# Optimization experiments

Measured on AMD Instinct MI355X. Metric: run time of the kernel, lower is better.

## Reference

```python
import jax, jax.numpy as jnp
import numpy as np

B, C, D, H, W = 1, 32, 48, 64, 208
EPS = 1e-5  # BatchNorm eps


def setup_inputs() -> dict:
    key = jax.random.key(0)
    ks = jax.random.split(key, 8)
    x = jax.random.normal(ks[0], (B, C, D, H, W), jnp.float32)
    g = jax.random.normal(ks[1], (B, 20, H, W), jnp.float32)
    conv_w = jax.random.normal(ks[2], (C, C, 3, 3, 3), jnp.float32) * 0.02
    bn1_gamma = 1.0 + 0.1 * jax.random.normal(ks[3], (C,), jnp.float32)
    bn1_beta = 0.1 * jax.random.normal(ks[4], (C,), jnp.float32)
    bn1_mean = 0.1 * jax.random.normal(ks[5], (C,), jnp.float32)
    bn1_var = jax.random.uniform(ks[6], (C,), jnp.float32, 0.5, 1.5)
    bn2_gamma = 1.0 + 0.1 * jax.random.normal(ks[7], (C,), jnp.float32)
    bn2_beta = jnp.zeros((C,), jnp.float32)
    bn2_mean = jnp.zeros((C,), jnp.float32)
    bn2_var = jnp.ones((C,), jnp.float32)
    return {
        'x': x, 'g': g, 'conv_w': conv_w,
        'bn1_gamma': bn1_gamma, 'bn1_beta': bn1_beta, 'bn1_mean': bn1_mean, 'bn1_var': bn1_var,
        'bn2_gamma': bn2_gamma, 'bn2_beta': bn2_beta, 'bn2_mean': bn2_mean, 'bn2_var': bn2_var,
    }


def _l1_normalize(k):
    # F.normalize(k, p=1, dim=1)
    return k / jnp.maximum(jnp.sum(jnp.abs(k), axis=1, keepdims=True), 1e-12)


def _sga_scan(x, w):
    """Directional semi-global aggregation along the LAST axis.
    x: [B,C,D,H,L] cost volume, w: [B,5,H,L] L1-normalized guidance weights.
    Recurrence (GANet SGA):
      A[p,d] = w0*x[p,d] + w1*A[p-1,d] + w2*A[p-1,d-1] + w3*A[p-1,d+1] + w4*max_d' A[p-1,d']
    """
    xs = jnp.moveaxis(x, -1, 0)  # [L,B,C,D,H]
    ws = jnp.moveaxis(w, -1, 0)  # [L,B,5,H]

    def step(prev, inp):
        xi, wi = inp  # [B,C,D,H], [B,5,H]
        w0, w1, w2, w3, w4 = [wi[:, i][:, None, None, :] for i in range(5)]
        up = jnp.concatenate([prev[:, :, :1], prev[:, :, :-1]], axis=2)   # A[d-1]
        dn = jnp.concatenate([prev[:, :, 1:], prev[:, :, -1:]], axis=2)   # A[d+1]
        mx = jnp.max(prev, axis=2, keepdims=True)                          # max_d A
        out = w0 * xi + w1 * prev + w2 * up + w3 * dn + w4 * mx
        return out, out

    _, outs = jax.lax.scan(step, xs[0], (xs, ws))  # boundary: carry init = raw cost slice
    return jnp.moveaxis(outs, 0, -1)


def _sga(x, k1, k2, k3, k4):
    # direction 1: left -> right (along W)
    d1 = _sga_scan(x, k1)
    # direction 2: right -> left
    d2 = jnp.flip(_sga_scan(jnp.flip(x, -1), jnp.flip(k2, -1)), -1)
    # vertical directions: swap H<->W so the scan axis is H
    xv = jnp.swapaxes(x, 3, 4)  # [B,C,D,W,H]
    d3 = jnp.swapaxes(_sga_scan(xv, jnp.swapaxes(k3, 2, 3)), 3, 4)  # top -> bottom
    d4 = jnp.swapaxes(
        jnp.flip(_sga_scan(jnp.flip(xv, -1), jnp.flip(jnp.swapaxes(k4, 2, 3), -1)), -1), 3, 4)
    # GANet combines directions with an elementwise max
    return jnp.maximum(jnp.maximum(d1, d2), jnp.maximum(d3, d4))


def _bn3d(x, gamma, beta, mean, var):
    s = (gamma / jnp.sqrt(var + EPS))[None, :, None, None, None]
    return (x - mean[None, :, None, None, None]) * s + beta[None, :, None, None, None]


def _conv3d_same(x, w):
    return jax.lax.conv_general_dilated(
        x, w, window_strides=(1, 1, 1), padding=[(1, 1)] * 3,
        dimension_numbers=('NCDHW', 'OIDHW', 'NCDHW'))


def reference(x, g, conv_w, bn1_gamma, bn1_beta, bn1_mean, bn1_var,
              bn2_gamma, bn2_beta, bn2_mean, bn2_var):
    rem = x
    k1, k2, k3, k4 = jnp.split(g, 4, axis=1)  # each [B,5,H,W]
    k1, k2, k3, k4 = map(_l1_normalize, (k1, k2, k3, k4))
    a = _sga(x, k1, k2, k3, k4)
    # refine=True branch: BN+ReLU then BasicConv(3x3x3, BN, no relu)
    a = jax.nn.relu(_bn3d(a, bn1_gamma, bn1_beta, bn1_mean, bn1_var))
    a = _conv3d_same(a, conv_w)
    a = _bn3d(a, bn2_gamma, bn2_beta, bn2_mean, bn2_var)
    return jax.nn.relu(a + rem)
```

## Files before the change

kernel.cpp:

```cpp
#include <hip/hip_runtime.h>
#include <hip/hip_bf16.h>
#include <cstddef>

#define C_ 32
#define D_ 48
#define DP_ 50
#define H_ 64
#define W_ 208
#define WP_ 210
#define HW_ 13312
#define HS_ 9984
#define EPS_ 1e-5f

typedef __attribute__((ext_vector_type(8))) short short8;
typedef __attribute__((ext_vector_type(4))) float float4v;
typedef __attribute__((ext_vector_type(16))) float float16v;
typedef __attribute__((ext_vector_type(2))) __fp16 half2v;

template<int CTRL>
__device__ __forceinline__ float dppmov(float x) {
    int v = __builtin_bit_cast(int, x);
    return __builtin_bit_cast(float,
        __builtin_amdgcn_update_dpp(v, v, CTRL, 0xf, 0xf, false));
}
template<int CTRL>
__device__ __forceinline__ float dppmax(float m) {
    return fmaxf(m, dppmov<CTRL>(m));
}
__device__ __forceinline__ float rl(float v, int idx) {
    return __builtin_bit_cast(float,
        __builtin_amdgcn_readlane(__builtin_bit_cast(int, v), idx));
}
template<int CTRL>
__device__ __forceinline__ unsigned dppu(unsigned x) {
    return (unsigned)__builtin_amdgcn_update_dpp((int)x, (int)x, CTRL, 0xf, 0xf, false);
}
__device__ __forceinline__ unsigned rlu(unsigned v, int idx) {
    return (unsigned)__builtin_amdgcn_readlane((int)v, idx);
}
__device__ __forceinline__ unsigned pkmax_u(unsigned a, unsigned b) {
    unsigned r;
    asm("v_pk_max_f16 %0, %1, %2" : "=v"(r) : "v"(a), "v"(b));
    return r;
}
__device__ __forceinline__ half2v hcast(unsigned u) { return __builtin_bit_cast(half2v, u); }
__device__ __forceinline__ unsigned ucast(half2v h) { return __builtin_bit_cast(unsigned, h); }

__device__ __forceinline__ unsigned sga_step_pk(unsigned Au, unsigned xiu,
    unsigned w0, unsigned w1, unsigned w2, unsigned w3, unsigned w4,
    bool actv, bool ge47)
{
    unsigned up = dppu<0x138>(Au);
    unsigned dn = dppu<0x130>(Au);
    dn = ge47 ? Au : dn;
    unsigned m = actv ? Au : 0xFBFFFBFFu;
    m = pkmax_u(m, dppu<0x111>(m));
    m = pkmax_u(m, dppu<0x112>(m));
    m = pkmax_u(m, dppu<0x114>(m));
    m = pkmax_u(m, dppu<0x118>(m));
    m = pkmax_u(m, dppu<0x142>(m));
    m = pkmax_u(m, dppu<0x143>(m));
    unsigned mall = rlu(m, 63);
    half2v A = hcast(Au), xi = hcast(xiu), uph = hcast(up), dnh = hcast(dn),
           mh = hcast(mall), h0 = hcast(w0), h1 = hcast(w1), h2 = hcast(w2),
           h3 = hcast(w3), h4 = hcast(w4);
    half2v r = (h0 * xi + h1 * A) + ((h2 * uph + h3 * dnh) + h4 * mh);
    return ucast(r);
}

__global__ __launch_bounds__(256) void prep_kernel(
    const float* __restrict__ g, const float* __restrict__ cw,
    float* __restrict__ wn, float* __restrict__ wnT,
    __hip_bfloat16* __restrict__ wrep, unsigned* __restrict__ actu)
{
    int idx = blockIdx.x * 256 + threadIdx.x;
    if (idx < 4 * HW_) {
        int dir = idx / HW_;
        int hw  = idx % HW_;
        const float* gb = g + dir * 5 * HW_ + hw;
        float v0 = gb[0*HW_], v1 = gb[1*HW_], v2 = gb[2*HW_], v3 = gb[3*HW_], v4 = gb[4*HW_];
        float s = fabsf(v0)+fabsf(v1)+fabsf(v2)+fabsf(v3)+fabsf(v4);
        float inv = 1.0f / fmaxf(s, 1e-12f);
        v0 *= inv; v1 *= inv; v2 *= inv; v3 *= inv; v4 *= inv;
        float* ob = wn + dir * 5 * HW_ + hw;
        ob[0*HW_] = v0; ob[1*HW_] = v1; ob[2*HW_] = v2; ob[3*HW_] = v3; ob[4*HW_] = v4;
        if (dir >= 2) {
            int hq = hw / W_, wq = hw % W_;
            float* oT = wnT + ((size_t)((dir-2)*5)*W_ + wq)*H_ + hq;
            oT[0]       = v0; oT[1*HW_] = v1; oT[2*HW_] = v2;
            oT[3*HW_]   = v3; oT[4*HW_] = v4;
        }
    } else if (idx < 4 * HW_ + 27648) {
        int j = idx - 4 * HW_;
        int e    = j & 7;
        int lane = (j >> 3) & 63;
        int q    = j >> 9;
        int cih  = q & 1;
        int tap  = q >> 1;
        int co = lane & 31;
        int ci = cih * 16 + (lane >> 5) * 8 + e;
        wrep[j] = __float2bfloat16(cw[(co * C_ + ci) * 27 + tap]);
    } else if (idx < 4 * HW_ + 27648 + 98304) {
        int j2 = idx - (4 * HW_ + 27648);
        int hd  = j2 >> 5;
        int r   = j2 & 31;
        int col = (r >> 4) ? 209 : 0;
        int cu  = r & 15;
        int h = hd / 48, dd = hd % 48;
        actu[(((size_t)h * DP_ + dd + 1) * WP_ + col) * 16 + cu] = 0u;
    } else {
        int j3 = idx - (4 * HW_ + 27648 + 98304);
        int pl   = j3 >= 215040;
        int r3   = pl ? j3 - 215040 : j3;
        int h    = r3 / 3360;
        int rest = r3 % 3360;
        int dpad = pl ? (DP_ - 1) : 0;
        actu[((size_t)h * DP_ + dpad) * WP_ * 16 + rest] = 0u;
    }
}

__global__ __launch_bounds__(256) void t0_kernel(
    const float* __restrict__ x, __hip_bfloat16* __restrict__ xt)
{
    __shared__ float t[48 * 257];
    int tid = threadIdx.x;
    int c  = blockIdx.x / 52;
    int q0 = (blockIdx.x % 52) * 256;
    #pragma unroll
    for (int dd = 0; dd < 48; ++dd)
        t[dd * 257 + tid] = x[((size_t)c * 48 + dd) * HW_ + q0 + tid];
    __syncthreads();
    unsigned* xtu = (unsigned*)xt;
    #pragma unroll
    for (int k = 0; k < 24; ++k) {
        int f = tid + 256 * k;
        int d2 = f % 24, hwl = f / 24;
        union { unsigned u; __hip_bfloat16 hh[2]; } pk;
        pk.hh[0] = __float2bfloat16(t[(2 * d2) * 257 + hwl]);
        pk.hh[1] = __float2bfloat16(t[(2 * d2 + 1) * 257 + hwl]);
        xtu[(((size_t)c * HW_ + q0 + hwl) * 48 + 2 * d2) >> 1] = pk.u;
    }
}

__global__ __launch_bounds__(128, 2) void sga_w_kernel(
    const __hip_bfloat16* __restrict__ xt, const float* __restrict__ wn,
    __hip_bfloat16* __restrict__ d12, unsigned* __restrict__ d1tmp)
{
    __shared__ unsigned sO[208][48];

    int lane = threadIdx.x & 63;
    int dir  = threadIdx.x >> 6;
    int pairI = blockIdx.x;
    int c  = pairI >> 5;
    int h0 = (pairI & 31) * 2;
    int d = lane < 48 ? lane : 47;
    bool actv = lane < 48, ge47 = lane >= 47;
    const __hip_bfloat16* xA = xt + ((size_t)c * HW_ + h0 * W_) * 48 + d;
    const __hip_bfloat16* xB = xA + HS_;
    const float* wbA = wn + (size_t)dir * 5 * HW_ + h0 * W_;
    int il = lane >> 3, jl = lane & 7;
    bool wact = il < 5;
    unsigned* tmpp = d1tmp + (size_t)pairI * 208 * 48 + d;

    unsigned xpk[3][8];
    unsigned wAr[3];

    if (dir == 0) {
        #pragma unroll
        for (int b = 0; b < 2; ++b) {
            #pragma unroll
            for (int j = 0; j < 8; ++j) {
                float fA = __bfloat162float(xA[(size_t)(b * 8 + j) * 48]);
                float fB = __bfloat162float(xB[(size_t)(b * 8 + j) * 48]);
                xpk[b][j] = ucast(__builtin_amdgcn_cvt_pkrtz(fA, fB));
            }
            float wfA = wact ? wbA[il * HW_ + b * 8 + jl] : 0.0f;
            float wfB = wact ? wbA[il * HW_ + W_ + b * 8 + jl] : 0.0f;
            wAr[b] = ucast(__builtin_amdgcn_cvt_pkrtz(wfA, wfB));
        }
        unsigned Au = xpk[0][0];
        #pragma unroll
        for (int cc = 0; cc < 26; ++cc) {
            const int buf = cc % 3;
            if (cc < 24) {
                const int nb = (cc + 2) % 3;
                #pragma unroll
                for (int j = 0; j < 8; ++j) {
                    float fA = __bfloat162float(xA[(size_t)((cc + 2) * 8 + j) * 48]);
                    float fB = __bfloat162float(xB[(size_t)((cc + 2) * 8 + j) * 48]);
                    xpk[nb][j] = ucast(__builtin_amdgcn_cvt_pkrtz(fA, fB));
                }
                float wfA = wact ? wbA[il * HW_ + (cc + 2) * 8 + jl] : 0.0f;
                float wfB = wact ? wbA[il * HW_ + W_ + (cc + 2) * 8 + jl] : 0.0f;
                wAr[nb] = ucast(__builtin_amdgcn_cvt_pkrtz(wfA, wfB));
            }
            #pragma unroll
            for (int j = 0; j < 8; ++j) {
                Au = sga_step_pk(Au, xpk[buf][j], rlu(wAr[buf], j), rlu(wAr[buf], 8 + j),
                                 rlu(wAr[buf], 16 + j), rlu(wAr[buf], 24 + j),
                                 rlu(wAr[buf], 32 + j), actv, ge47);
                if (actv) tmpp[(size_t)(cc * 8 + j) * 48] = Au;
            }
        }
    } else {
        #pragma unroll
        for (int b = 0; b < 2; ++b) {
            const int base = 200 - b * 8;
            #pragma unroll
            for (int j = 0; j < 8; ++j) {
                float fA = __bfloat162float(xA[(size_t)(base + j) * 48]);
                float fB = __bfloat162float(xB[(size_t)(base + j) * 48]);
                xpk[b][j] = ucast(__builtin_amdgcn_cvt_pkrtz(fA, fB));
            }
            float wfA = wact ? wbA[il * HW_ + base + jl] : 0.0f;
            float wfB = wact ? wbA[il * HW_ + W_ + base + jl] : 0.0f;
            wAr[b] = ucast(__builtin_amdgcn_cvt_pkrtz(wfA, wfB));
        }
        unsigned Au = xpk[0][7];
        #pragma unroll
        for (int cc2 = 0; cc2 < 26; ++cc2) {
            const int cc = 25 - cc2;
            const int buf = cc2 % 3;
            if (cc2 < 24) {
                const int nb = (cc2 + 2) % 3;
                #pragma unroll
                for (int j = 0; j < 8; ++j) {
                    float fA = __bfloat162float(xA[(size_t)((cc - 2) * 8 + j) * 48]);
                    float fB = __bfloat162float(xB[(size_t)((cc - 2) * 8 + j) * 48]);
                    xpk[nb][j] = ucast(__builtin_amdgcn_cvt_pkrtz(fA, fB));
                }
                float wfA = wact ? wbA[il * HW_ + (cc - 2) * 8 + jl] : 0.0f;
                float wfB = wact ? wbA[il * HW_ + W_ + (cc - 2) * 8 + jl] : 0.0f;
                wAr[nb] = ucast(__builtin_amdgcn_cvt_pkrtz(wfA, wfB));
            }
            #pragma unroll
            for (int j = 7; j >= 0; --j) {
                Au = sga_step_pk(Au, xpk[buf][j], rlu(wAr[buf], j), rlu(wAr[buf], 8 + j),
                                 rlu(wAr[buf], 16 + j), rlu(wAr[buf], 24 + j),
                                 rlu(wAr[buf], 32 + j), actv, ge47);
                if (actv) sO[cc * 8 + j][d] = Au;
            }
        }
    }

    __syncthreads();

    __hip_bfloat16* dpA = d12 + ((size_t)c * HW_ + h0 * W_) * 48 + d;
    __hip_bfloat16* dpB = dpA + HS_;
    if (actv) {
        const int p0 = dir * 104;
        #pragma unroll 8
        for (int t = 0; t < 104; ++t) {
            int p = p0 + t;
            unsigned um = pkmax_u(tmpp[(size_t)p * 48], sO[p][d]);
            half2v mh = hcast(um);
            dpA[(size_t)p * 48] = __float2bfloat16((float)mh[0]);
            dpB[(size_t)p * 48] = __float2bfloat16((float)mh[1]);
        }
    }
}

__global__ __launch_bounds__(128, 3) void sga_h_kernel(
    const __hip_bfloat16* __restrict__ xt, const float* __restrict__ wnT,
    __hip_bfloat16* __restrict__ d12,
    const float* __restrict__ g1, const float* __restrict__ b1,
    const float* __restrict__ m1, const float* __restrict__ v1)
{
    __shared__ unsigned sO[2][64][48];

    int lane = threadIdx.x & 63;
    int dir  = threadIdx.x >> 6;
    int gp   = blockIdx.x;
    int g0 = gp * 2;
    int c = g0 / W_, w = g0 % W_;
    int d = lane < 48 ? lane : 47;
    bool actv = lane < 48, ge47 = lane >= 47;
    const __hip_bfloat16* xA = xt + ((size_t)c * HW_ + w) * 48 + d;
    const __hip_bfloat16* xB = xA + 48;
    const float* wbA = wnT + ((size_t)(dir * 5) * W_ + w) * H_;
    const float* wbB = wbA + H_;
    int il = lane >> 3, jl = lane & 7;
    bool wact = il < 5;

    unsigned xpk[3][8];
    unsigned wAr[3];

    if (dir == 0) {
        #pragma unroll
        for (int b = 0; b < 2; ++b) {
            #pragma unroll
            for (int j = 0; j < 8; ++j) {
                float fA = __bfloat162float(xA[(size_t)(b * 8 + j) * HS_]);
                float fB = __bfloat162float(xB[(size_t)(b * 8 + j) * HS_]);
                xpk[b][j] = ucast(__builtin_amdgcn_cvt_pkrtz(fA, fB));
            }
            float wfA = wact ? wbA[il * HW_ + b * 8 + jl] : 0.0f;
            float wfB = wact ? wbB[il * HW_ + b * 8 + jl] : 0.0f;
            wAr[b] = ucast(__builtin_amdgcn_cvt_pkrtz(wfA, wfB));
        }
        unsigned Au = xpk[0][0];
        #pragma unroll
        for (int cc = 0; cc < 8; ++cc) {
            const int buf = cc % 3;
            if (cc < 6) {
                const int nb = (cc + 2) % 3;
                #pragma unroll
                for (int j = 0; j < 8; ++j) {
                    float fA = __bfloat162float(xA[(size_t)((cc + 2) * 8 + j) * HS_]);
                    float fB = __bfloat162float(xB[(size_t)((cc + 2) * 8 + j) * HS_]);
                    xpk[nb][j] = ucast(__builtin_amdgcn_cvt_pkrtz(fA, fB));
                }
                float wfA = wact ? wbA[il * HW_ + (cc + 2) * 8 + jl] : 0.0f;
                float wfB = wact ? wbB[il * HW_ + (cc + 2) * 8 + jl] : 0.0f;
                wAr[nb] = ucast(__builtin_amdgcn_cvt_pkrtz(wfA, wfB));
            }
            #pragma unroll
            for (int j = 0; j < 8; ++j) {
                Au = sga_step_pk(Au, xpk[buf][j], rlu(wAr[buf], j), rlu(wAr[buf], 8 + j),
                                 rlu(wAr[buf], 16 + j), rlu(wAr[buf], 24 + j),
                                 rlu(wAr[buf], 32 + j), actv, ge47);
                if (actv) sO[0][cc * 8 + j][d] = Au;
            }
        }
    } else {
        #pragma unroll
        for (int b = 0; b < 2; ++b) {
            const int base = 56 - b * 8;
            #pragma unroll
            for (int j = 0; j < 8; ++j) {
                float fA = __bfloat162float(xA[(size_t)(base + j) * HS_]);
                float fB = __bfloat162float(xB[(size_t)(base + j) * HS_]);
                xpk[b][j] = ucast(__builtin_amdgcn_cvt_pkrtz(fA, fB));
            }
            float wfA = wact ? wbA[il * HW_ + base + jl] : 0.0f;
            float wfB = wact ? wbB[il * HW_ + base + jl] : 0.0f;
            wAr[b] = ucast(__builtin_amdgcn_cvt_pkrtz(wfA, wfB));
        }
        unsigned Au = xpk[0][7];
        #pragma unroll
        for (int cc2 = 0; cc2 < 8; ++cc2) {
            const int cc = 7 - cc2;
            const int buf = cc2 % 3;
            if (cc2 < 6) {
                const int nb = (cc2 + 2) % 3;
                #pragma unroll
                for (int j = 0; j < 8; ++j) {
                    float fA = __bfloat162float(xA[(size_t)((cc - 2) * 8 + j) * HS_]);
                    float fB = __bfloat162float(xB[(size_t)((cc - 2) * 8 + j) * HS_]);
                    xpk[nb][j] = ucast(__builtin_amdgcn_cvt_pkrtz(fA, fB));
                }
                float wfA = wact ? wbA[il * HW_ + (cc - 2) * 8 + jl] : 0.0f;
                float wfB = wact ? wbB[il * HW_ + (cc - 2) * 8 + jl] : 0.0f;
                wAr[nb] = ucast(__builtin_amdgcn_cvt_pkrtz(wfA, wfB));
            }
            #pragma unroll
            for (int j = 7; j >= 0; --j) {
                Au = sga_step_pk(Au, xpk[buf][j], rlu(wAr[buf], j), rlu(wAr[buf], 8 + j),
                                 rlu(wAr[buf], 16 + j), rlu(wAr[buf], 24 + j),
                                 rlu(wAr[buf], 32 + j), actv, ge47);
                if (actv) sO[1][cc * 8 + j][d] = Au;
            }
        }
    }

    __syncthreads();

    float s1 = g1[c] * rsqrtf(v1[c] + EPS_);
    float o1 = b1[c] - m1[c] * s1;
    __hip_bfloat16* dpA = d12 + ((size_t)c * HW_ + w) * 48 + d;
    __hip_bfloat16* dpB = dpA + 48;
    #pragma unroll
    for (int t = 0; t < 32; ++t) {
        int h = dir * 32 + t;
        unsigned um = pkmax_u(sO[0][h][d], sO[1][h][d]);
        half2v mh = hcast(um);
        if (actv) {
            float vA = fmaxf((float)mh[0], __bfloat162float(dpA[(size_t)h * HS_]));
            float vB = fmaxf((float)mh[1], __bfloat162float(dpB[(size_t)h * HS_]));
            dpA[(size_t)h * HS_] = __float2bfloat16(fmaxf(vA * s1 + o1, 0.0f));
            dpB[(size_t)h * HS_] = __float2bfloat16(fmaxf(vB * s1 + o1, 0.0f));
        }
    }
}

__global__ __launch_bounds__(256) void trans_kernel(
    const __hip_bfloat16* __restrict__ st, __hip_bfloat16* __restrict__ act)
{
    __shared__ float t[8 * 1571];
    int tid = threadIdx.x;
    int h  = blockIdx.x / 26;
    int w0 = (blockIdx.x % 26) * 8;
    const unsigned* stu = (const unsigned*)st;
    #pragma unroll
    for (int k = 0; k < 24; ++k) {
        int f = tid + 256 * k;
        int d2 = f % 24, wl = (f / 24) % 8, c = f / 192;
        unsigned u = stu[(((size_t)c * HW_ + h * W_ + w0 + wl) * 48 + 2 * d2) >> 1];
        const __hip_bfloat16* bp = (const __hip_bfloat16*)&u;
        t[wl * 1571 + c * 49 + 2 * d2]     = __bfloat162float(bp[0]);
        t[wl * 1571 + c * 49 + 2 * d2 + 1] = __bfloat162float(bp[1]);
    }
    __syncthreads();
    unsigned* actu = (unsigned*)act;
    #pragma unroll
    for (int k = 0; k < 24; ++k) {
        int f = tid + 256 * k;
        int cp = f % 16, wl = (f / 16) % 8, d = f / 128;
        union { unsigned u; __hip_bfloat16 hh[2]; } pk;
        pk.hh[0] = __float2bfloat16(t[wl * 1571 + (2 * cp) * 49 + d]);
        pk.hh[1] = __float2bfloat16(t[wl * 1571 + (2 * cp + 1) * 49 + d]);
        actu[(((size_t)h * DP_ + d + 1) * WP_ + w0 + wl + 1) * 16 + cp] = pk.u;
    }
}

__global__ __launch_bounds__(256, 4) void conv_kernel(
    const __hip_bfloat16* __restrict__ act,
    const short8* __restrict__ wrep,
    const float* __restrict__ x,
    const float* __restrict__ g2, const float* __restrict__ b2,
    const float* __restrict__ m2, const float* __restrict__ v2,
    float* __restrict__ out)
{
    __shared__ __hip_bfloat16 sAct[10 * 34 * 40];

    int tid  = threadIdx.x;
    int lane = tid & 63;
    int v    = tid >> 6;
    int bid  = blockIdx.x;
    int wt   = bid % 7;
    int t    = bid / 7;
    int h    = t & 63;
    int d0b  = (t >> 6) * 8;
    int w0   = wt * 32;
    int n    = lane & 31;
    int half = lane >> 5;

    float16v acc0 = (float16v)(0.0f);
    float16v acc1 = (float16v)(0.0f);

    const short8* ap8 = (const short8*)act;

    #pragma unroll
    for (int kh = 0; kh < 3; ++kh) {
        int hh = h + kh - 1;
        if (hh < 0 || hh >= H_) continue;
        __syncthreads();
        #pragma unroll
        for (int k = 0; k < 6; ++k) {
            int i = tid + 256 * k;
            if (i < 1360) {
                int dp = i / 136;
                int r  = i - dp * 136;
                int wl = r >> 2, q = r & 3;
                int wc = w0 + wl; wc = wc < 209 ? wc : 209;
                short8 vd = ap8[(((size_t)hh * DP_ + d0b + dp) * WP_ + wc) * 4 + q];
                *(short8*)&sAct[(dp * 34 + wl) * 40 + q * 8] = vd;
            }
        }
        __syncthreads();
        #pragma unroll
        for (int kw = 0; kw < 3; ++kw) {
            #pragma unroll
            for (int cih = 0; cih < 2; ++cih) {
                short8 af[3];
                #pragma unroll
                for (int kd = 0; kd < 3; ++kd)
                    af[kd] = wrep[(((kd*3 + kh)*3 + kw)*2 + cih)*64 + lane];
                short8 bf[4];
                #pragma unroll
                for (int p = 0; p < 4; ++p)
                    bf[p] = *(const short8*)
                        &sAct[((2*v + p) * 34 + kw + n) * 40 + cih * 16 + half * 8];
                #pragma unroll
                for (int kd = 0; kd < 3; ++kd) {
                    acc0 = __builtin_amdgcn_mfma_f32_32x32x16_bf16(af[kd], bf[kd],   acc0, 0, 0, 0);
                    acc1 = __builtin_amdgcn_mfma_f32_32x32x16_bf16(af[kd], bf[kd+1], acc1, 0, 0, 0);
                }
            }
        }
    }

    int d0 = d0b + 2 * v;
    int wl = w0 + n;
    bool wvalid = wl < W_;
    int coh = 4 * half;
    #pragma unroll
    for (int r = 0; r < 16; ++r) {
        int co = (r & 3) + 8 * (r >> 2) + coh;
        float s2 = g2[co] * rsqrtf(v2[co] + EPS_);
        float o2 = b2[co] - m2[co] * s2;
        size_t idx0 = ((size_t)(co * D_ + d0) * H_ + h) * W_ + wl;
        if (wvalid) {
            out[idx0]       = fmaxf(acc0[r] * s2 + o2 + x[idx0],       0.0f);
            out[idx0 + HW_] = fmaxf(acc1[r] * s2 + o2 + x[idx0 + HW_], 0.0f);
        }
    }
}

extern "C" void kernel_launch(void* const* d_in, const int* in_sizes, int n_in,
                              void* d_out, int out_size, void* d_ws, size_t ws_size,
                              hipStream_t stream)
{
    const float* x    = (const float*)d_in[0];
    const float* g    = (const float*)d_in[1];
    const float* cw   = (const float*)d_in[2];
    const float* bn1g = (const float*)d_in[3];
    const float* bn1b = (const float*)d_in[4];
    const float* bn1m = (const float*)d_in[5];
    const float* bn1v = (const float*)d_in[6];
    const float* bn2g = (const float*)d_in[7];
    const float* bn2b = (const float*)d_in[8];
    const float* bn2m = (const float*)d_in[9];
    const float* bn2v = (const float*)d_in[10];
    float* out = (float*)d_out;

    char* ws = (char*)d_ws;
    float* wn  = (float*)ws;
    float* wnT = (float*)(ws + 1064960);
    __hip_bfloat16* wrep = (__hip_bfloat16*)(ws + 1597440);
    __hip_bfloat16* d12t = (__hip_bfloat16*)(ws + 1652736);
    __hip_bfloat16* act  = (__hip_bfloat16*)(ws + 42547200);
    __hip_bfloat16* xt = (__hip_bfloat16*)out;
    unsigned* d1tmp = (unsigned*)((char*)out + 40894464);

    prep_kernel<<<2380, 256, 0, stream>>>(g, cw, wn, wnT, wrep, (unsigned*)act);
    t0_kernel<<<1664, 256, 0, stream>>>(x, xt);
    sga_w_kernel<<<1024, 128, 0, stream>>>(xt, wn, d12t, d1tmp);
    sga_h_kernel<<<3328, 128, 0, stream>>>(xt, wnT, d12t, bn1g, bn1b, bn1m, bn1v);
    trans_kernel<<<1664, 256, 0, stream>>>(d12t, act);
    conv_kernel<<<2688, 256, 0, stream>>>(act, (const short8*)wrep, x,
                                          bn2g, bn2b, bn2m, bn2v, out);
}
```

Before: 382.8 us.

## Prefetch next kh activation slice into registers and reduce LDS row padding

The conv kernel now loads the next kh row of activations from global memory into registers while the MFMAs for the current row run. After a barrier it writes that row to shared memory, which hides global-load latency behind compute. The shared-memory row stride also drops from 40 to 36 bf16, shrinking LDS use and changing the bank-conflict pattern. The register staging adds about 24 VGPRs, which may pressure the occupancy target of 4 blocks.

```diff
diff --git a/kernel.cpp b/kernel.cpp
--- a/kernel.cpp
+++ b/kernel.cpp
@@ -11,6 +11,7 @@
 #define HW_ 13312
 #define HS_ 9984
 #define EPS_ 1e-5f
+#define LPAD_ 36
 
 typedef __attribute__((ext_vector_type(8))) short short8;
 typedef __attribute__((ext_vector_type(4))) float float4v;
@@ -421,7 +422,7 @@
     const float* __restrict__ m2, const float* __restrict__ v2,
     float* __restrict__ out)
 {
-    __shared__ __hip_bfloat16 sAct[10 * 34 * 40];
+    __shared__ __hip_bfloat16 sAct[10 * 34 * LPAD_];
 
     int tid  = threadIdx.x;
     int lane = tid & 63;
@@ -440,24 +441,47 @@
 
     const short8* ap8 = (const short8*)act;
 
-    #pragma unroll
-    for (int kh = 0; kh < 3; ++kh) {
-        int hh = h + kh - 1;
-        if (hh < 0 || hh >= H_) continue;
-        __syncthreads();
-        #pragma unroll
-        for (int k = 0; k < 6; ++k) {
-            int i = tid + 256 * k;
-            if (i < 1360) {
-                int dp = i / 136;
-                int r  = i - dp * 136;
-                int wl = r >> 2, q = r & 3;
-                int wc = w0 + wl; wc = wc < 209 ? wc : 209;
-                short8 vd = ap8[(((size_t)hh * DP_ + d0b + dp) * WP_ + wc) * 4 + q];
-                *(short8*)&sAct[(dp * 34 + wl) * 40 + q * 8] = vd;
-            }
-        }
-        __syncthreads();
+    int sdp[6], swl[6], sq[6];
+    #pragma unroll
+    for (int k = 0; k < 6; ++k) {
+        int i = tid + 256 * k;
+        sdp[k] = i / 136;
+        int r = i - sdp[k] * 136;
+        swl[k] = r >> 2; sq[k] = r & 3;
+    }
+    short8 stg[6];
+
+    int hh0 = (h > 0) ? h - 1 : 0;
+    int hh1 = (h < H_ - 1) ? h + 1 : H_ - 1;
+
+    #pragma unroll
+    for (int k = 0; k < 6; ++k) {
+        int i = tid + 256 * k;
+        if (i < 1360) {
+            int wc = w0 + swl[k]; wc = wc < 209 ? wc : 209;
+            stg[k] = ap8[(((size_t)hh0 * DP_ + d0b + sdp[k]) * WP_ + wc) * 4 + sq[k]];
+        }
+    }
+    #pragma unroll
+    for (int k = 0; k < 6; ++k) {
+        int i = tid + 256 * k;
+        if (i < 1360)
+            *(short8*)&sAct[(sdp[k] * 34 + swl[k]) * LPAD_ + sq[k] * 8] = stg[k];
+    }
+    __syncthreads();
+
+    for (int hh = hh0; hh <= hh1; ++hh) {
+        int kh = hh - h + 1;
+        if (hh < hh1) {
+            #pragma unroll
+            for (int k = 0; k < 6; ++k) {
+                int i = tid + 256 * k;
+                if (i < 1360) {
+                    int wc = w0 + swl[k]; wc = wc < 209 ? wc : 209;
+                    stg[k] = ap8[(((size_t)(hh + 1) * DP_ + d0b + sdp[k]) * WP_ + wc) * 4 + sq[k]];
+                }
+            }
+        }
         #pragma unroll
         for (int kw = 0; kw < 3; ++kw) {
             #pragma unroll
@@ -470,13 +494,23 @@
                 #pragma unroll
                 for (int p = 0; p < 4; ++p)
                     bf[p] = *(const short8*)
-                        &sAct[((2*v + p) * 34 + kw + n) * 40 + cih * 16 + half * 8];
+                        &sAct[((2*v + p) * 34 + kw + n) * LPAD_ + cih * 16 + half * 8];
                 #pragma unroll
                 for (int kd = 0; kd < 3; ++kd) {
                     acc0 = __builtin_amdgcn_mfma_f32_32x32x16_bf16(af[kd], bf[kd],   acc0, 0, 0, 0);
                     acc1 = __builtin_amdgcn_mfma_f32_32x32x16_bf16(af[kd], bf[kd+1], acc1, 0, 0, 0);
                 }
             }
+        }
+        __syncthreads();
+        if (hh < hh1) {
+            #pragma unroll
+            for (int k = 0; k < 6; ++k) {
+                int i = tid + 256 * k;
+                if (i < 1360)
+                    *(short8*)&sAct[(sdp[k] * 34 + swl[k]) * LPAD_ + sq[k] * 8] = stg[k];
+            }
+            __syncthreads();
         }
     }
 
```

After: 599.4 us. 56.6% more time.
